# Kernel tuning notes

Hardware: AMD Instinct MI355X
Metric: run time of the kernel (lower is better)

Reference implementation:

```python
import jax, jax.numpy as jnp
import numpy as np

K = 20
IN_CH = 128
OUT_CH = 128


def setup_inputs() -> dict:
    key = jax.random.key(0)
    k1, k2, k3, k4, k5, k6 = jax.random.split(key, 6)
    B, N = 2, 8192
    pos = jax.random.normal(k1, (B, N, 3), dtype=jnp.float32)
    features = jax.random.normal(k2, (B, N, IN_CH), dtype=jnp.float32)
    # fc = Linear(2C -> OUT) , ReLU, Linear(OUT -> OUT); stored as [in, out]
    s1 = 1.0 / np.sqrt(2 * IN_CH)
    s2 = 1.0 / np.sqrt(OUT_CH)
    W1 = jax.random.uniform(k3, (2 * IN_CH, OUT_CH), jnp.float32, -s1, s1)
    b1 = jax.random.uniform(k4, (OUT_CH,), jnp.float32, -s1, s1)
    W2 = jax.random.uniform(k5, (OUT_CH, OUT_CH), jnp.float32, -s2, s2)
    b2 = jax.random.uniform(k6, (OUT_CH,), jnp.float32, -s2, s2)
    return {"pos": pos, "features": features, "W1": W1, "b1": b1, "W2": W2, "b2": b2}


def reference(pos, features, W1, b1, W2, b2):
    B, N, _ = pos.shape
    C = features.shape[-1]
    p = pos.reshape(-1, 3)            # [BN, 3] (cross-batch, as in original)
    f = features.reshape(-1, C)       # [BN, C]
    # squared pairwise distances (same top-k ordering as torch.cdist)
    sq = jnp.sum(p * p, axis=-1)
    d2 = sq[:, None] + sq[None, :] - 2.0 * (p @ p.T)   # [BN, BN]
    _, knn_idx = jax.lax.top_k(-d2, K)                 # [BN, K] smallest dists
    nb = f[knn_idx]                                    # [BN, K, C] gather
    center = jnp.broadcast_to(f[:, None, :], nb.shape)
    edge = jnp.concatenate([center, nb - center], axis=-1)   # [BN, K, 2C]
    h = jax.nn.relu(jnp.einsum('nkc,cd->nkd', edge, W1) + b1)
    h = jnp.einsum('nkd,de->nke', h, W2) + b2          # [BN, K, OUT]
    x = jnp.max(h, axis=1)                             # max aggregation
    return x.reshape(B, N, -1)
```

## Files before the change

kernel.cpp:

```cpp
#include <hip/hip_runtime.h>

typedef unsigned short u16;
typedef unsigned int   u32;
typedef unsigned long long u64;
typedef short s16x8 __attribute__((ext_vector_type(8)));
typedef float f32x4 __attribute__((ext_vector_type(4)));

#define NPTS   16384
#define KNNK   20
#define SLOTS3 12
#define TRIG3  4
#define NSEG   16
#define PSZ    1024
#define SCAP   24

#define MFMA_BF16 __builtin_amdgcn_mfma_f32_16x16x32_bf16

__device__ __forceinline__ u16 f2bf(float x) {
  u32 u = __builtin_bit_cast(u32, x);
  u32 r = (u + 0x7FFFu + ((u >> 16) & 1u)) >> 16;
  return (u16)r;
}
__device__ __forceinline__ float bf2f(u16 b) {
  u32 u = ((u32)b) << 16;
  return __builtin_bit_cast(float, u);
}
__device__ __forceinline__ float dist2(float4 qp, float4 cd) {
  float dot = fmaf(qp.x, cd.x, fmaf(qp.y, cd.y, qp.z * cd.z));
  return fmaf(-2.0f, dot, qp.w + cd.w);
}

__global__ __launch_bounds__(256) void knnconv_prep(const float* __restrict__ pos,
                                                    float4* __restrict__ pos4) {
  int i = blockIdx.x * 256 + threadIdx.x;
  float x = pos[i * 3 + 0], y = pos[i * 3 + 1], z = pos[i * 3 + 2];
  float sq = (x * x + y * y) + z * z;
  pos4[i] = make_float4(x, y, z, sq);
}

__global__ __launch_bounds__(1024) void knnconv_s0(const float4* __restrict__ pos4,
                                                   float* __restrict__ tau) {
  __shared__ float sd[SLOTS3 * 1024];
  __shared__ float md[16][64][4];
  const int tid  = threadIdx.x;
  const int lane = tid & 63;
  const int wv   = __builtin_amdgcn_readfirstlane(tid >> 6);
  const int qg   = blockIdx.x;
  const int q    = qg * 64 + lane;
  const float4 qp = pos4[q];
  const float INF = __builtin_inff();

  float t0v = INF, t1v = INF, t2v = INF;
  float thrF = INF;
  int cnt = 0;
  const int kbase = wv * 256;

#define FLUSH3()                                                      \
  { _Pragma("unroll 1")                                               \
    for (int e = 0; e < SLOTS3; e += 2) {                             \
      if (!__any(e < cnt)) break;                                     \
      float lo = (e     < cnt) ? sd[e * 1024 + tid]       : INF;      \
      float hi = (e + 1 < cnt) ? sd[(e + 1) * 1024 + tid] : INF;      \
      float a_ = fminf(lo, hi), b_ = fmaxf(lo, hi);                   \
      lo = a_; hi = b_;                                               \
      { float m = fminf(lo, t0v), x = fmaxf(lo, t0v);                 \
        t0v = m; lo = fminf(x, hi); hi = fmaxf(x, hi); }              \
      { float m = fminf(lo, t1v), x = fmaxf(lo, t1v);                 \
        t1v = m; lo = fminf(x, hi); hi = fmaxf(x, hi); }              \
      t2v = fminf(lo, t2v);                                           \
    }                                                                 \
    thrF = t2v;                                                       \
    cnt = 0; }

  for (int t0 = 0; t0 < 256; t0 += 8) {
    float4 g[8];
    #pragma unroll
    for (int u = 0; u < 8; ++u) g[u] = pos4[(kbase + t0 + u) * 4];
    #pragma unroll
    for (int u = 0; u < 8; ++u) {
      float d2 = dist2(qp, g[u]);
      sd[cnt * 1024 + tid] = d2;
      cnt += (d2 < thrF) ? 1 : 0;
    }
    if (__any(cnt >= TRIG3)) { FLUSH3(); }
  }
  FLUSH3();

  md[wv][lane][0] = t0v;
  md[wv][lane][1] = t1v;
  md[wv][lane][2] = t2v;
  md[wv][lane][3] = INF;
  __syncthreads();

  if (tid < 64) {
    int ql = tid;
    int h0=0,h1=0,h2=0,h3=0,h4=0,h5=0,h6=0,h7=0;
    int h8=0,h9=0,h10=0,h11=0,h12=0,h13=0,h14=0,h15=0;
    float last = INF;
    for (int r = 0; r < KNNK; ++r) {
      float c0 = md[ 0][ql][h0],  c1 = md[ 1][ql][h1];
      float c2 = md[ 2][ql][h2],  c3 = md[ 3][ql][h3];
      float c4 = md[ 4][ql][h4],  c5 = md[ 5][ql][h5];
      float c6 = md[ 6][ql][h6],  c7 = md[ 7][ql][h7];
      float c8 = md[ 8][ql][h8],  c9 = md[ 9][ql][h9];
      float cA = md[10][ql][h10], cB = md[11][ql][h11];
      float cC = md[12][ql][h12], cD = md[13][ql][h13];
      float cE = md[14][ql][h14], cF = md[15][ql][h15];
      float bv = c0; int bw = 0;
      if (c1 < bv) { bv = c1; bw = 1; }
      if (c2 < bv) { bv = c2; bw = 2; }
      if (c3 < bv) { bv = c3; bw = 3; }
      if (c4 < bv) { bv = c4; bw = 4; }
      if (c5 < bv) { bv = c5; bw = 5; }
      if (c6 < bv) { bv = c6; bw = 6; }
      if (c7 < bv) { bv = c7; bw = 7; }
      if (c8 < bv) { bv = c8; bw = 8; }
      if (c9 < bv) { bv = c9; bw = 9; }
      if (cA < bv) { bv = cA; bw = 10; }
      if (cB < bv) { bv = cB; bw = 11; }
      if (cC < bv) { bv = cC; bw = 12; }
      if (cD < bv) { bv = cD; bw = 13; }
      if (cE < bv) { bv = cE; bw = 14; }
      if (cF < bv) { bv = cF; bw = 15; }
      last = bv;
      h0  += (bw==0);  h1  += (bw==1);  h2  += (bw==2);  h3  += (bw==3);
      h4  += (bw==4);  h5  += (bw==5);  h6  += (bw==6);  h7  += (bw==7);
      h8  += (bw==8);  h9  += (bw==9);  h10 += (bw==10); h11 += (bw==11);
      h12 += (bw==12); h13 += (bw==13); h14 += (bw==14); h15 += (bw==15);
    }
    tau[qg * 64 + ql] = last * 1.00001f;
  }
}

__global__ __launch_bounds__(256) void knnconv_s1x(const float4* __restrict__ pos4,
                                                   const float* __restrict__ tau,
                                                   u16* __restrict__ g1,
                                                   u16* __restrict__ gcnt) {
  const int tid  = threadIdx.x;
  const int lane = tid & 63;
  const int wv   = __builtin_amdgcn_readfirstlane(tid >> 6);
  const int qg   = blockIdx.x >> 2;
  const int pb   = blockIdx.x & 3;
  const int part = pb * 4 + wv;
  const int q    = qg * 64 + lane;
  const float4 P = pos4[q];
  const float Qx = P.x, Qy = P.y, Qz = P.z;
  const float Qt = 0.5f * (tau[q] - P.w);
  const int cbase = part * PSZ;
  const float4* cp = pos4 + cbase;
  u16* seg = g1 + (q * NSEG + part) * SCAP;
  int cnt = 0;

  #pragma unroll 1
  for (int t0 = 0; t0 < PSZ; t0 += 8) {
    float4 c[8];
    #pragma unroll
    for (int u = 0; u < 8; ++u) c[u] = cp[t0 + u];
    #pragma unroll
    for (int u = 0; u < 8; ++u) {
      float dot = fmaf(Qx, c[u].x, fmaf(Qy, c[u].y, Qz * c[u].z));
      float lhs = fmaf(0.5f, c[u].w, -dot);
      if (lhs <= Qt) {
        if (cnt < SCAP) seg[cnt] = (u16)(cbase + t0 + u);
        ++cnt;
      }
    }
  }
  gcnt[q * NSEG + part] = (u16)min(cnt, SCAP);
}

__global__ __launch_bounds__(256) void knnconv_s2(const float4* __restrict__ pos4,
                                                  const u16* __restrict__ g1,
                                                  const u16* __restrict__ gcnt,
                                                  u16* __restrict__ knn_out) {
  __shared__ u64 keys[16 * 256];
  __shared__ int Tq[16];
  const int tid = threadIdx.x;
  const int iq = tid >> 4, s = tid & 15;
  const int q0 = blockIdx.x * 16;
  const int q = q0 + iq;

  #pragma unroll
  for (int i = 0; i < 16; ++i) keys[i * 256 + tid] = ~0ULL;
  __syncthreads();

  int off = 0, T = 0;
  #pragma unroll
  for (int j = 0; j < NSEG; ++j) {
    int cj = gcnt[q * NSEG + j];
    off += (j < s) ? cj : 0;
    T += cj;
  }
  if (s == 15) Tq[iq] = min(T, 256);
  int myc = gcnt[q * NSEG + s];
  float4 P = pos4[q];
  for (int i = 0; i < myc; ++i) {
    int pos = off + i;
    if (pos >= 256) break;
    int cidx = (int)g1[(q * NSEG + s) * SCAP + i];
    float4 C = pos4[cidx];
    double qx = P.x, qy = P.y, qz = P.z;
    double cx = C.x, cy = C.y, cz = C.z;
    double sqq = qx * qx + qy * qy + qz * qz;
    double sqc = cx * cx + cy * cy + cz * cz;
    double dot = qx * cx + qy * cy + qz * cz;
    double d   = (sqq + sqc) - 2.0 * dot;
    float df = fmaxf((float)d, 0.0f);
    keys[iq * 256 + pos] = ((u64)__builtin_bit_cast(u32, df) << 14) | (u32)cidx;
  }
  __syncthreads();

  #pragma unroll 1
  for (int t = 0; t < 16; ++t) {
    int T2 = Tq[t];
    if (tid < T2) {
      u64 kj = keys[t * 256 + tid];
      const u64* row = keys + t * 256;
      int r = 0;
      for (int k = 0; k < T2; ++k) r += (row[k] < kj) ? 1 : 0;
      if (r < KNNK)
        knn_out[(q0 + t) * KNNK + r] = (u16)(kj & 0x3FFFu);
    }
  }
}

__global__ __launch_bounds__(256) void knnconv_wprep(const float* __restrict__ W1,
                                                     const float* __restrict__ W2,
                                                     u16* __restrict__ w1bf,
                                                     u16* __restrict__ w2bf) {
  int b = blockIdx.x;
  if (b < 128) {
    int e = b * 256 + threadIdx.x;
    int n = e >> 7, kk = e & 127;
    float v;
    if (n < 128) v = W1[(128 + kk) * 128 + n];
    else { int n2 = n - 128; v = W1[kk * 128 + n2] - W1[(128 + kk) * 128 + n2]; }
    w1bf[(n * 256 + ((kk * 2) ^ ((n & 7) << 4))) >> 1] = f2bf(v);
  } else {
    int e = (b - 128) * 256 + threadIdx.x;
    int n = e >> 7, kk = e & 127;
    w2bf[(n * 256 + ((kk * 2) ^ ((n & 7) << 4))) >> 1] = f2bf(W2[kk * 128 + n]);
  }
}

__global__ __launch_bounds__(256) void knnconv_prec(const float* __restrict__ feat,
                                                    const u16* __restrict__ w1bf,
                                                    const float* __restrict__ b1,
                                                    u16* __restrict__ a_out,
                                                    float* __restrict__ c_out) {
  __shared__ char sW[65536];
  __shared__ char sF[16384];
  const int tid = threadIdx.x;
  {
    const uint4* src = (const uint4*)w1bf;
    uint4* dst = (uint4*)sW;
    #pragma unroll
    for (int r = 0; r < 16; ++r) dst[r * 256 + tid] = src[r * 256 + tid];
  }
  {
    int sub = tid & 15, r0 = tid >> 4;
    int m0 = blockIdx.x * 64;
    for (int rr = 0; rr < 4; ++rr) {
      int r = r0 + rr * 16;
      const float* src = feat + (m0 + r) * 128 + sub * 8;
      float4 v0 = *(const float4*)src;
      float4 v1 = *(const float4*)(src + 4);
      u32 p0 = (u32)f2bf(v0.x) | ((u32)f2bf(v0.y) << 16);
      u32 p1 = (u32)f2bf(v0.z) | ((u32)f2bf(v0.w) << 16);
      u32 p2 = (u32)f2bf(v1.x) | ((u32)f2bf(v1.y) << 16);
      u32 p3 = (u32)f2bf(v1.z) | ((u32)f2bf(v1.w) << 16);
      *(uint4*)(sF + r * 256 + ((sub * 16) ^ ((r & 7) << 4))) = make_uint4(p0, p1, p2, p3);
    }
  }
  __syncthreads();
  const int lane = tid & 63, wv = tid >> 6;
  const int l15 = lane & 15, l4 = lane >> 4;
  f32x4 acc[4][4];
  #pragma unroll
  for (int a = 0; a < 4; ++a)
    #pragma unroll
    for (int b = 0; b < 4; ++b) acc[a][b] = (f32x4){0.f, 0.f, 0.f, 0.f};
  #pragma unroll
  for (int kk = 0; kk < 4; ++kk) {
    int kb = kk * 64 + l4 * 16;
    s16x8 af[4], bfr[4];
    #pragma unroll
    for (int mt = 0; mt < 4; ++mt) {
      int row = mt * 16 + l15;
      af[mt] = *(const s16x8*)(sF + row * 256 + (kb ^ ((row & 7) << 4)));
    }
    #pragma unroll
    for (int nt = 0; nt < 4; ++nt) {
      int n = (wv * 4 + nt) * 16 + l15;
      bfr[nt] = *(const s16x8*)(sW + n * 256 + (kb ^ ((n & 7) << 4)));
    }
    #pragma unroll
    for (int mt = 0; mt < 4; ++mt)
      #pragma unroll
      for (int nt = 0; nt < 4; ++nt)
        acc[mt][nt] = MFMA_BF16(af[mt], bfr[nt], acc[mt][nt], 0, 0, 0);
  }
  int m0 = blockIdx.x * 64;
  #pragma unroll
  for (int nt = 0; nt < 4; ++nt) {
    int n = (wv * 4 + nt) * 16 + l15;
    float bias = (n >= 128) ? b1[n - 128] : 0.0f;
    #pragma unroll
    for (int mt = 0; mt < 4; ++mt)
      #pragma unroll
      for (int r = 0; r < 4; ++r) {
        int m = m0 + mt * 16 + l4 * 4 + r;
        float v = acc[mt][nt][r];
        if (n < 128) a_out[m * 128 + n] = f2bf(v);
        else         c_out[m * 128 + (n - 128)] = v + bias;
      }
  }
}

__global__ __launch_bounds__(256) void knnconv_conv(const u16* __restrict__ knn,
                                                    const u16* __restrict__ a_in,
                                                    const float* __restrict__ c_in,
                                                    const u16* __restrict__ w2bf,
                                                    const float* __restrict__ b2,
                                                    float* __restrict__ out) {
  __shared__ char lds[77824];
  char* sA = lds;
  char* sW = lds + 40960;
  char* sC = lds + 73728;
  const int tid = threadIdx.x;
  const int q0 = blockIdx.x * 8;

  {
    int row = tid >> 5, ch4 = (tid & 31) * 4;
    *(float4*)(sC + (row * 128 + ch4) * 4) = *(const float4*)(c_in + (q0 + row) * 128 + ch4);
  }
  __syncthreads();
  {
    const uint4* src = (const uint4*)w2bf;
    uint4* dst = (uint4*)sW;
    #pragma unroll
    for (int r = 0; r < 8; ++r) dst[r * 256 + tid] = src[r * 256 + tid];
  }
  {
    int sub = tid & 15, rr = tid >> 4;
    for (int p = 0; p < 10; ++p) {
      int r = p * 16 + rr;
      int il = r / 20;
      int ke = r - il * 20;
      int idx = (int)knn[(q0 + il) * KNNK + ke];
      uint4 av = *(const uint4*)(a_in + idx * 128 + sub * 8);
      float4 c0 = *(const float4*)(sC + (il * 128 + sub * 8) * 4);
      float4 c1 = *(const float4*)(sC + (il * 128 + sub * 8 + 4) * 4);
      float h0 = fmaxf(bf2f((u16)(av.x & 0xFFFF)) + c0.x, 0.f);
      float h1 = fmaxf(bf2f((u16)(av.x >> 16))    + c0.y, 0.f);
      float h2 = fmaxf(bf2f((u16)(av.y & 0xFFFF)) + c0.z, 0.f);
      float h3 = fmaxf(bf2f((u16)(av.y >> 16))    + c0.w, 0.f);
      float h4 = fmaxf(bf2f((u16)(av.z & 0xFFFF)) + c1.x, 0.f);
      float h5 = fmaxf(bf2f((u16)(av.z >> 16))    + c1.y, 0.f);
      float h6 = fmaxf(bf2f((u16)(av.w & 0xFFFF)) + c1.z, 0.f);
      float h7 = fmaxf(bf2f((u16)(av.w >> 16))    + c1.w, 0.f);
      u32 p0 = (u32)f2bf(h0) | ((u32)f2bf(h1) << 16);
      u32 p1 = (u32)f2bf(h2) | ((u32)f2bf(h3) << 16);
      u32 p2 = (u32)f2bf(h4) | ((u32)f2bf(h5) << 16);
      u32 p3 = (u32)f2bf(h6) | ((u32)f2bf(h7) << 16);
      *(uint4*)(sA + r * 256 + ((sub * 16) ^ ((r & 7) << 4))) = make_uint4(p0, p1, p2, p3);
    }
  }
  __syncthreads();
  const int lane = tid & 63, wv = tid >> 6;
  const int l15 = lane & 15, l4 = lane >> 4;
  f32x4 acc[10][2];
  #pragma unroll
  for (int mt = 0; mt < 10; ++mt) { acc[mt][0] = (f32x4){0,0,0,0}; acc[mt][1] = (f32x4){0,0,0,0}; }
  #pragma unroll
  for (int kk = 0; kk < 4; ++kk) {
    int kb = kk * 64 + l4 * 16;
    s16x8 b0, b1r;
    { int n = (wv * 2 + 0) * 16 + l15; b0  = *(const s16x8*)(sW + n * 256 + (kb ^ ((n & 7) << 4))); }
    { int n = (wv * 2 + 1) * 16 + l15; b1r = *(const s16x8*)(sW + n * 256 + (kb ^ ((n & 7) << 4))); }
    #pragma unroll
    for (int mt = 0; mt < 10; ++mt) {
      int row = mt * 16 + l15;
      s16x8 a = *(const s16x8*)(sA + row * 256 + (kb ^ ((row & 7) << 4)));
      acc[mt][0] = MFMA_BF16(a, b0,  acc[mt][0], 0, 0, 0);
      acc[mt][1] = MFMA_BF16(a, b1r, acc[mt][1], 0, 0, 0);
    }
  }
  __syncthreads();
  #pragma unroll
  for (int mt = 0; mt < 10; ++mt)
    #pragma unroll
    for (int nt = 0; nt < 2; ++nt) {
      int n = (wv * 2 + nt) * 16 + l15;
      #pragma unroll
      for (int r = 0; r < 4; ++r) {
        int row = mt * 16 + l4 * 4 + r;
        *(u16*)(sA + row * 256 + n * 2) = f2bf(acc[mt][nt][r]);
      }
    }
  __syncthreads();
  {
    int ch = tid & 127, g = tid >> 7;
    float bias = b2[ch];
    for (int pp = 0; pp < 4; ++pp) {
      int qq = pp * 2 + g;
      float mx = -__builtin_inff();
      #pragma unroll
      for (int e = 0; e < KNNK; ++e)
        mx = fmaxf(mx, bf2f(*(const u16*)(sA + (qq * 20 + e) * 256 + ch * 2)));
      out[(q0 + qq) * 128 + ch] = mx + bias;
    }
  }
}

extern "C" void kernel_launch(void* const* d_in, const int* in_sizes, int n_in,
                              void* d_out, int out_size, void* d_ws, size_t ws_size,
                              hipStream_t stream) {
  const float* pos  = (const float*)d_in[0];
  const float* feat = (const float*)d_in[1];
  const float* W1   = (const float*)d_in[2];
  const float* b1   = (const float*)d_in[3];
  const float* W2   = (const float*)d_in[4];
  const float* b2   = (const float*)d_in[5];
  float* out = (float*)d_out;
  char* ws = (char*)d_ws;
  float4* pos4  = (float4*)ws;
  u16*    w1bf  = (u16*)ws;
  u16*    w2bf  = (u16*)(ws + 65536);
  u16*    knn   = (u16*)(ws + 262144);
  u16*    g1    = (u16*)(ws + 917504);
  u16*    a_buf = (u16*)(ws + 917504);
  float*  c_buf = (float*)(ws + 5111808);
  u16*    gcnt  = (u16*)(ws + 13500416);
  float*  tau   = (float*)(ws + 14024704);
  if (ws_size < 14090240) return;

  knnconv_prep<<<64, 256, 0, stream>>>(pos, pos4);
  knnconv_s0<<<256, 1024, 0, stream>>>(pos4, tau);
  knnconv_s1x<<<1024, 256, 0, stream>>>(pos4, tau, g1, gcnt);
  knnconv_s2<<<1024, 256, 0, stream>>>(pos4, g1, gcnt, knn);
  knnconv_wprep<<<192, 256, 0, stream>>>(W1, W2, w1bf, w2bf);
  knnconv_prec<<<256, 256, 0, stream>>>(feat, w1bf, b1, a_buf, c_buf);
  knnconv_conv<<<2048, 256, 0, stream>>>(knn, a_buf, c_buf, w2bf, b2, out);
}
```

Baseline: 226.6 us.

## Transpose kNN filter pass: lanes over candidates, ballot-compacted writes per query

The candidate filter kernel now assigns lanes to candidate points and loops over the 64 queries held in shared memory. Before, each lane owned one query and scanned candidates serially. Accepted candidates are found with a wave ballot, compacted with popcount prefix offsets, and written contiguously, with the per-query count kept in the owning lane. Candidate loads are coalesced and prefetched two windows ahead. The cost is a ballot/shuffle per query per window, and correctness depends on acceptance order matching the old serial scan.

Result: slower. 252.9 us (+11.6%).

```diff
diff --git a/kernel.cpp b/kernel.cpp
--- a/kernel.cpp
+++ b/kernel.cpp
@@ -136,37 +136,56 @@
                                                    const float* __restrict__ tau,
                                                    u16* __restrict__ g1,
                                                    u16* __restrict__ gcnt) {
+  __shared__ float4 sQ[64];
   const int tid  = threadIdx.x;
   const int lane = tid & 63;
-  const int wv   = __builtin_amdgcn_readfirstlane(tid >> 6);
+  const int wv   = tid >> 6;
   const int qg   = blockIdx.x >> 2;
   const int pb   = blockIdx.x & 3;
   const int part = pb * 4 + wv;
-  const int q    = qg * 64 + lane;
-  const float4 P = pos4[q];
-  const float Qx = P.x, Qy = P.y, Qz = P.z;
-  const float Qt = 0.5f * (tau[q] - P.w);
+  const int qbase = qg * 64;
+  if (tid < 64) {
+    float4 P = pos4[qbase + tid];
+    sQ[tid] = make_float4(P.x, P.y, P.z, 0.5f * (tau[qbase + tid] - P.w));
+  }
+  __syncthreads();
+
   const int cbase = part * PSZ;
-  const float4* cp = pos4 + cbase;
-  u16* seg = g1 + (q * NSEG + part) * SCAP;
   int cnt = 0;
 
+#define S1WIN(CD, W)                                                  \
+  { const float cx_ = CD.x, cy_ = CD.y, cz_ = CD.z;                   \
+    const float cw2_ = 0.5f * CD.w;                                   \
+    _Pragma("unroll 16")                                              \
+    for (int j = 0; j < 64; ++j) {                                    \
+      float4 Q = sQ[j];                                               \
+      float dot = fmaf(Q.x, cx_, fmaf(Q.y, cy_, Q.z * cz_));          \
+      bool acc = (cw2_ - dot) <= Q.w;                                 \
+      u64 mask = __ballot(acc);                                       \
+      if (mask) {                            \
+        int base = __shfl(cnt, j);                                    \
+        int pc = __popcll(mask);                                      \
+        if (acc) {                                                    \
+          int slot = base + __popcll(mask & ((1ULL << lane) - 1));    \
+          if (slot < SCAP)                                            \
+            g1[((qbase + j) * NSEG + part) * SCAP + slot] =           \
+                (u16)(cbase + (W) * 64 + lane);                       \
+        }                                                             \
+        cnt += (lane == j) ? pc : 0;                                  \
+      }                                                               \
+    } }
+
+  float4 A = pos4[cbase + 0 * 64 + lane];
+  float4 B = pos4[cbase + 1 * 64 + lane];
   #pragma unroll 1
-  for (int t0 = 0; t0 < PSZ; t0 += 8) {
-    float4 c[8];
-    #pragma unroll
-    for (int u = 0; u < 8; ++u) c[u] = cp[t0 + u];
-    #pragma unroll
-    for (int u = 0; u < 8; ++u) {
-      float dot = fmaf(Qx, c[u].x, fmaf(Qy, c[u].y, Qz * c[u].z));
-      float lhs = fmaf(0.5f, c[u].w, -dot);
-      if (lhs <= Qt) {
-        if (cnt < SCAP) seg[cnt] = (u16)(cbase + t0 + u);
-        ++cnt;
-      }
-    }
-  }
-  gcnt[q * NSEG + part] = (u16)min(cnt, SCAP);
+  for (int w = 0; w < 16; w += 2) {
+    float4 nA = pos4[cbase + min(w + 2, 15) * 64 + lane];
+    S1WIN(A, w);
+    float4 nB = pos4[cbase + min(w + 3, 15) * 64 + lane];
+    S1WIN(B, w + 1);
+    A = nA; B = nB;
+  }
+  gcnt[(qbase + lane) * NSEG + part] = (u16)min(cnt, SCAP);
 }
 
 __global__ __launch_bounds__(256) void knnconv_s2(const float4* __restrict__ pos4,
```
